# Performance work log

Hardware: AMD Instinct MI355X
Metric: run time of the kernel (lower is better)

The kernel has to match this reference:

```python
import jax, jax.numpy as jnp
import numpy as np
import math

B, L, D, H = 2, 2048, 1024, 16
DH = D // H
TAU = 1.0
EPS_LN = 1e-12


def neural_sort(scores, tau=TAU):
    # scores: (B, n) -> soft permutation P_hat: (B, n, n)
    s = scores[..., None]                                   # (B,n,1)
    A = jnp.abs(s - jnp.swapaxes(s, 1, 2))                  # (B,n,n) pairwise |s_i - s_j|
    Bsum = jnp.sum(A, axis=-1, keepdims=True)               # row sums == A @ ones(n,n) columns
    n = scores.shape[-1]
    scaling = (n + 1 - 2 * (jnp.arange(n) + 1)).astype(scores.dtype)  # (n,)
    C = s * scaling[None, None, :]                          # (B,n,n)
    P_max = jnp.swapaxes(C - Bsum, 1, 2)
    return jax.nn.softmax(P_max / tau, axis=-1)


def euler_transform(v, delta, b_euler, log_scale, is_query):
    # v: (B,L,D); soft-sort channels, polar decompose, rotate, recompose
    Bv, Lv, Dv = v.shape
    scores = v.mean(axis=1)                                 # (B,D)
    P = neural_sort(scores)                                 # (B,D,D)
    v_sorted = jnp.einsum('bij,blj->bli', P, v)             # permute channel dim
    r, p = v_sorted[..., ::2], v_sorted[..., 1::2]          # (B,L,D/2)
    lam = jnp.sqrt(r * r + p * p + 1e-6)
    lam_d = jax.lax.stop_gradient(lam)
    theta = jnp.arctan2(p / lam_d, r / lam_d)
    theta = theta * delta
    if is_query:
        theta = theta + b_euler
    lam = lam * jnp.exp(jnp.clip(log_scale, -5.0, 5.0))
    out = jnp.stack([lam * jnp.cos(theta), lam * jnp.sin(theta)], axis=-1)
    return out.reshape(Bv, Lv, Dv)


def layer_norm(x, gamma, beta, eps=EPS_LN):
    mu = x.mean(axis=-1, keepdims=True)
    var = ((x - mu) ** 2).mean(axis=-1, keepdims=True)
    return (x - mu) / jnp.sqrt(var + eps) * gamma + beta


def forward(input_tensor, Wq, bq, Wk, bk, Wv, bv, Wd, bd, gamma, beta, delta, b_euler, log_scale):
    q = input_tensor @ Wq.T + bq
    k = input_tensor @ Wk.T + bk
    v = input_tensor @ Wv.T + bv
    q = euler_transform(q, delta, b_euler, log_scale, is_query=True)
    k = euler_transform(k, delta, b_euler, log_scale, is_query=False)
    def heads(x):
        return x.reshape(B, L, H, DH).transpose(0, 2, 1, 3)  # (B,H,L,DH)
    qh, kh, vh = heads(q), heads(k), heads(v)
    scores = jnp.einsum('bhqd,bhkd->bhqk', qh, kh) / math.sqrt(DH)
    probs = jax.nn.softmax(scores, axis=-1)                 # dropout off (eval)
    ctx = jnp.einsum('bhqk,bhkd->bhqd', probs, vh)
    ctx = ctx.transpose(0, 2, 1, 3).reshape(B, L, D)
    hidden = ctx @ Wd.T + bd
    return layer_norm(hidden + input_tensor, gamma, beta)


def setup_inputs() -> dict:
    key = jax.random.key(0)
    ks = jax.random.split(key, 16)
    s = 1.0 / math.sqrt(D)
    return {
        'input_tensor': jax.random.normal(ks[0], (B, L, D), jnp.float32),
        'Wq': jax.random.normal(ks[1], (D, D), jnp.float32) * s,
        'bq': jnp.zeros((D,), jnp.float32),
        'Wk': jax.random.normal(ks[2], (D, D), jnp.float32) * s,
        'bk': jnp.zeros((D,), jnp.float32),
        'Wv': jax.random.normal(ks[3], (D, D), jnp.float32) * s,
        'bv': jnp.zeros((D,), jnp.float32),
        'Wd': jax.random.normal(ks[4], (D, D), jnp.float32) * s,
        'bd': jnp.zeros((D,), jnp.float32),
        'gamma': jnp.ones((D,), jnp.float32),
        'beta': jnp.zeros((D,), jnp.float32),
        'delta': jnp.full((1, 1, D // 2), 0.1, jnp.float32),
        'b_euler': jnp.zeros((1, 1, D // 2), jnp.float32),
        'log_scale': jnp.zeros((1, 1, D // 2), jnp.float32),
    }


def reference(input_tensor, Wq, bq, Wk, bk, Wv, bv, Wd, bd, gamma, beta, delta, b_euler, log_scale):
    return forward(input_tensor, Wq, bq, Wk, bk, Wv, bv, Wd, bd, gamma, beta, delta, b_euler, log_scale)
```

## Files before the change

kernel.cpp:

```cpp
#include <hip/hip_runtime.h>


typedef unsigned short bf16_t;
typedef short frag_ab __attribute__((ext_vector_type(8)));
typedef float frag_cd __attribute__((ext_vector_type(4)));

#define BB 2
#define LL 2048
#define DD 1024
#define HH 16
#define DH 64

#define QSCALE 0.18033688f
#define EOFF  -17.3123404907f

__device__ __forceinline__ float b2f(bf16_t u) {
  union { unsigned int i; float f; } c; c.i = ((unsigned int)u) << 16; return c.f;
}
__device__ __forceinline__ bf16_t f2b(float f) {
  union { float f; unsigned int i; } c; c.f = f;
  unsigned int r = c.i + 0x7fffu + ((c.i >> 16) & 1u);
  return (bf16_t)(r >> 16);
}
__device__ __forceinline__ unsigned int fbits(float f) {
  union { float f; unsigned int i; } c; c.f = f; return c.i;
}
__device__ __forceinline__ float tr16(float x) {
  union { float f; unsigned int i; } c; c.f = x; c.i &= 0xffff0000u; return c.f;
}
__device__ __forceinline__ float waveMax(float v) {
#pragma unroll
  for (int m = 32; m > 0; m >>= 1) v = fmaxf(v, __shfl_xor(v, m));
  return v;
}
__device__ __forceinline__ float waveSum(float v) {
#pragma unroll
  for (int m = 32; m > 0; m >>= 1) v += __shfl_xor(v, m);
  return v;
}

__device__ __forceinline__ void gll16(const bf16_t* g, bf16_t* l) {
  __builtin_amdgcn_global_load_lds(
      (const __attribute__((address_space(1))) void*)g,
      (__attribute__((address_space(3))) void*)l, 16, 0, 0);
}

__device__ __forceinline__ frag_ab ld_tile(const bf16_t* base, int row, int chunk) {
  return *(const frag_ab*)((const char*)base + (row << 7) + (((chunk ^ row) & 7) << 4));
}

__global__ __launch_bounds__(256) void prep_cast(const float* __restrict__ X,
                                                 const float* __restrict__ Wv,
                                                 const float* __restrict__ Wd,
                                                 bf16_t* __restrict__ Xb,
                                                 bf16_t* __restrict__ Wvb,
                                                 bf16_t* __restrict__ Wdb,
                                                 float* __restrict__ xmean) {
  const int bid = blockIdx.x;
  if (bid == 6144) {
    if (threadIdx.x < 256)
      for (int i = threadIdx.x; i < BB * DD; i += 256) xmean[i] = 0.f;
    return;
  }
  const float* in;
  bf16_t* out;
  int i;
  if (bid < 4096)      { in = X;  out = Xb;  i = bid * 256 + threadIdx.x; }
  else if (bid < 5120) { in = Wv; out = Wvb; i = (bid - 4096) * 256 + threadIdx.x; }
  else                 { in = Wd; out = Wdb; i = (bid - 5120) * 256 + threadIdx.x; }
  float4 v = ((const float4*)in)[i];
  ushort4 o;
  o.x = f2b(v.x); o.y = f2b(v.y); o.z = f2b(v.z); o.w = f2b(v.w);
  ((ushort4*)out)[i] = o;
}

__global__ __launch_bounds__(256) void cast_transpose_w(const float* __restrict__ Wq,
                                                        const float* __restrict__ Wk,
                                                        bf16_t* __restrict__ WqT,
                                                        bf16_t* __restrict__ WkT) {
  const float* W = blockIdx.z ? Wk : Wq;
  bf16_t* WT = blockIdx.z ? WkT : WqT;
  __shared__ bf16_t T[64][72];
  const int i0 = blockIdx.x * 64, m0 = blockIdx.y * 64;
  const int tid = threadIdx.x;
#pragma unroll
  for (int it = 0; it < 4; ++it) {
    const int idx = tid + it * 256;
    const int r = idx >> 4, c4 = (idx & 15) * 4;
    float4 v = *(const float4*)&W[(size_t)(i0 + r) * DD + m0 + c4];
    T[c4 + 0][r] = f2b(v.x);
    T[c4 + 1][r] = f2b(v.y);
    T[c4 + 2][r] = f2b(v.z);
    T[c4 + 3][r] = f2b(v.w);
  }
  __syncthreads();
#pragma unroll
  for (int it = 0; it < 2; ++it) {
    const int idx = tid + it * 256;
    const int r = idx >> 3, seg = idx & 7;
    *(uint4*)&WT[(size_t)(m0 + r) * DD + i0 + seg * 8] = *(const uint4*)&T[r][seg * 8];
  }
}

struct GemmB { const bf16_t* A; const bf16_t* Bm; const float* bias; float* Cf; bf16_t* Cb; };
struct GemmArgs { GemmB gb[6]; };

__global__ __launch_bounds__(256) void gemm128(GemmArgs ga, int M, int N, int K) {
  const GemmB g = ga.gb[blockIdx.z];
  const int bm = blockIdx.y * 128, bn = blockIdx.x * 128;
  __shared__ bf16_t As[128][32];
  __shared__ bf16_t Bs[128][32];
  bf16_t* As_f = &As[0][0];
  bf16_t* Bs_f = &Bs[0][0];
  const int tid = threadIdx.x;
  const int lane = tid & 63, w = tid >> 6;
  const int quad = lane >> 4, l16 = lane & 15;
  const int wm = (w >> 1) * 64, wn = (w & 1) * 64;
  const int wbase = w << 9;

  frag_cd acc[4][4];
#pragma unroll
  for (int i = 0; i < 4; ++i)
#pragma unroll
    for (int j = 0; j < 4; ++j)
#pragma unroll
      for (int r = 0; r < 4; ++r) acc[i][j][r] = 0.f;

  const int r0 = tid >> 2, s0 = (tid & 3) * 8;
  const int r1 = (tid + 256) >> 2, s1 = ((tid + 256) & 3) * 8;
  const size_t aoff0 = (size_t)(bm + r0) * K + s0;
  const size_t aoff1 = (size_t)(bm + r1) * K + s1;
  const size_t boff0 = (size_t)(bn + r0) * K + s0;
  const size_t boff1 = (size_t)(bn + r1) * K + s1;

  for (int k0 = 0; k0 < K; k0 += 32) {
    __syncthreads();
    gll16(g.A + aoff0 + k0, As_f + wbase);
    gll16(g.A + aoff1 + k0, As_f + 2048 + wbase);
    gll16(g.Bm + boff0 + k0, Bs_f + wbase);
    gll16(g.Bm + boff1 + k0, Bs_f + 2048 + wbase);
    __syncthreads();
    frag_ab af[4], bfr[4];
#pragma unroll
    for (int i = 0; i < 4; ++i) {
      af[i]  = *(const frag_ab*)&As[wm + i * 16 + l16][quad * 8];
      bfr[i] = *(const frag_ab*)&Bs[wn + i * 16 + l16][quad * 8];
    }
#pragma unroll
    for (int i = 0; i < 4; ++i)
#pragma unroll
      for (int j = 0; j < 4; ++j)
        acc[i][j] = __builtin_amdgcn_mfma_f32_16x16x32_bf16(af[i], bfr[j], acc[i][j], 0, 0, 0);
  }

#pragma unroll
  for (int i = 0; i < 4; ++i) {
#pragma unroll
    for (int r = 0; r < 4; ++r) {
      const int row = bm + wm + i * 16 + quad * 4 + r;
#pragma unroll
      for (int j = 0; j < 4; ++j) {
        const int col = bn + wn + j * 16 + l16;
        float v = acc[i][j][r];
        if (g.bias) v += g.bias[col];
        if (g.Cf) g.Cf[(size_t)row * N + col] = v;
        if (g.Cb) g.Cb[(size_t)row * N + col] = f2b(v);
      }
    }
  }
}

__global__ __launch_bounds__(256) void gemm64x64(GemmArgs ga, int M, int N, int K) {
  const GemmB g = ga.gb[blockIdx.z];
  const int bm = blockIdx.y * 64, bn = blockIdx.x * 64;
  __shared__ bf16_t As[64][32];
  __shared__ bf16_t Bs[64][32];
  bf16_t* As_f = &As[0][0];
  bf16_t* Bs_f = &Bs[0][0];
  const int tid = threadIdx.x;
  const int lane = tid & 63, w = tid >> 6;
  const int quad = lane >> 4, l16 = lane & 15;
  const int wm = (w >> 1) * 32, wn = (w & 1) * 32;
  const int wbase = w << 9;

  frag_cd acc[2][2];
#pragma unroll
  for (int i = 0; i < 2; ++i)
#pragma unroll
    for (int j = 0; j < 2; ++j)
#pragma unroll
      for (int r = 0; r < 4; ++r) acc[i][j][r] = 0.f;

  const int r0 = tid >> 2, s0 = (tid & 3) * 8;
  const size_t aoff0 = (size_t)(bm + r0) * K + s0;
  const size_t boff0 = (size_t)(bn + r0) * K + s0;

  for (int k0 = 0; k0 < K; k0 += 32) {
    __syncthreads();
    gll16(g.A + aoff0 + k0, As_f + wbase);
    gll16(g.Bm + boff0 + k0, Bs_f + wbase);
    __syncthreads();
    frag_ab af[2], bfr[2];
#pragma unroll
    for (int i = 0; i < 2; ++i) {
      af[i]  = *(const frag_ab*)&As[wm + i * 16 + l16][quad * 8];
      bfr[i] = *(const frag_ab*)&Bs[wn + i * 16 + l16][quad * 8];
    }
#pragma unroll
    for (int i = 0; i < 2; ++i)
#pragma unroll
      for (int j = 0; j < 2; ++j)
        acc[i][j] = __builtin_amdgcn_mfma_f32_16x16x32_bf16(af[i], bfr[j], acc[i][j], 0, 0, 0);
  }

#pragma unroll
  for (int i = 0; i < 2; ++i) {
#pragma unroll
    for (int r = 0; r < 4; ++r) {
      const int row = bm + wm + i * 16 + quad * 4 + r;
#pragma unroll
      for (int j = 0; j < 2; ++j) {
        const int col = bn + wn + j * 16 + l16;
        float v = acc[i][j][r];
        if (g.bias) v += g.bias[col];
        if (g.Cf) g.Cf[(size_t)row * N + col] = v;
        if (g.Cb) g.Cb[(size_t)row * N + col] = f2b(v);
      }
    }
  }
}

__global__ __launch_bounds__(256) void xmean_kernel(const float* __restrict__ X,
                                                    float* __restrict__ xmean) {
  const int d = blockIdx.x * 256 + threadIdx.x;
  const int b = blockIdx.z;
  const int l0 = blockIdx.y * 64;
  float s = 0.f;
  for (int l = l0; l < l0 + 64; ++l)
    s += X[((size_t)b * LL + l) * DD + d];
  atomicAdd(&xmean[b * DD + d], s * (1.f / (float)LL));
}

__global__ __launch_bounds__(256) void scores_gemm(const float* __restrict__ xmean,
                                                   const float* __restrict__ Wq,
                                                   const float* __restrict__ bq,
                                                   const float* __restrict__ Wk,
                                                   const float* __restrict__ bk,
                                                   float* __restrict__ scores) {
  const int w = threadIdx.x >> 6, lane = threadIdx.x & 63;
  const int idx = blockIdx.x * 4 + w;
  const int t = idx >> 11, b = (idx >> 10) & 1, i = idx & 1023;
  const float* W = t ? Wk : Wq;
  const float* bias = t ? bk : bq;
  const float* xm = xmean + b * DD;
  float sum = 0.f;
#pragma unroll
  for (int k = 0; k < 4; ++k) {
    float4 wv = *(const float4*)&W[(size_t)i * DD + k * 256 + lane * 4];
    float4 xv = *(const float4*)&xm[k * 256 + lane * 4];
    sum += wv.x * xv.x + wv.y * xv.y + wv.z * xv.z + wv.w * xv.w;
  }
  sum = waveSum(sum);
  if (lane == 0) scores[idx] = sum + bias[i];
}

__global__ __launch_bounds__(256) void bsum_kernel(const float* __restrict__ scores,
                                                   float* __restrict__ bsum) {
  __shared__ float sc[DD];
  const int z = blockIdx.x, jb = blockIdx.y, tid = threadIdx.x;
#pragma unroll
  for (int s = 0; s < 4; ++s) sc[tid + s * 256] = scores[z * DD + tid + s * 256];
  __syncthreads();
  const int j = jb * 256 + tid;
  const float si = sc[j];
  float s = 0.f;
  for (int m = 0; m < DD; m += 4) {
    float4 v = *(const float4*)&sc[m];
    s += fabsf(si - v.x) + fabsf(si - v.y) + fabsf(si - v.z) + fabsf(si - v.w);
  }
  bsum[z * DD + j] = s;
}

__global__ __launch_bounds__(256) void p_kernel(const float* __restrict__ scores,
                                                const float* __restrict__ bsum,
                                                const float* __restrict__ bq,
                                                const float* __restrict__ bk,
                                                bf16_t* __restrict__ Pq,
                                                bf16_t* __restrict__ Pk,
                                                float* __restrict__ bias4) {
  const int i = blockIdx.x;
  const int z = blockIdx.y;
  const int t = z >> 1, b = z & 1;
  const float* sc = scores + z * DD;
  const float* bs = bsum + z * DD;
  const float* bias = t ? bk : bq;
  const float scal = 1023.f - 2.f * (float)i;
  const int tid = threadIdx.x;
  __shared__ float redA[4], redB[4], redC[4];

  float lg[4], bb[4];
  float mx = -1e30f;
#pragma unroll
  for (int s = 0; s < 4; ++s) {
    const int j = tid + s * 256;
    lg[s] = sc[j] * scal - bs[j];
    bb[s] = bias[j];
    mx = fmaxf(mx, lg[s]);
  }
  mx = waveMax(mx);
  if ((tid & 63) == 0) redA[tid >> 6] = mx;
  __syncthreads();
  const float M = fmaxf(fmaxf(redA[0], redA[1]), fmaxf(redA[2], redA[3]));
  float sum = 0.f, dot = 0.f;
#pragma unroll
  for (int s = 0; s < 4; ++s) {
    lg[s] = __expf(lg[s] - M);
    sum += lg[s];
    dot += lg[s] * bb[s];
  }
  sum = waveSum(sum); dot = waveSum(dot);
  if ((tid & 63) == 0) { redB[tid >> 6] = sum; redC[tid >> 6] = dot; }
  __syncthreads();
  const float inv = 1.f / (redB[0] + redB[1] + redB[2] + redB[3]);
  bf16_t* P = (t ? Pk : Pq) + ((size_t)b << 20) + (size_t)i * DD;
#pragma unroll
  for (int s = 0; s < 4; ++s) P[tid + s * 256] = f2b(lg[s] * inv);
  if (tid == 0)
    bias4[t * 2048 + b * 1024 + i] = (redC[0] + redC[1] + redC[2] + redC[3]) * inv;
}

__global__ __launch_bounds__(256) void euler_transv(bf16_t* __restrict__ qs,
                                                    bf16_t* __restrict__ ks,
                                                    const float* __restrict__ delta,
                                                    const float* __restrict__ beul,
                                                    const float* __restrict__ lsc,
                                                    const bf16_t* __restrict__ vb,
                                                    bf16_t* __restrict__ vbT) {
  __shared__ bf16_t T[64][72];
  const int bid = blockIdx.x;
  const int tid = threadIdx.x;
  if (bid < 16384) {
    const int isq = (bid < 8192);
    unsigned int* buf = (unsigned int*)(isq ? qs : ks);
    const int idx = (isq ? bid : bid - 8192) * 256 + tid;
    const int c = idx & 511;
    const size_t n = idx >> 9;
    const unsigned int u = buf[n * 512 + c];
    const float r = b2f((bf16_t)(u & 0xffffu));
    const float p = b2f((bf16_t)(u >> 16));
    float lam = sqrtf(r * r + p * p + 1e-6f);
    float th = atan2f(p, r) * delta[c];
    if (isq) th += beul[c];
    lam *= __expf(fminf(fmaxf(lsc[c], -5.f), 5.f));
    if (isq) lam *= QSCALE;
    float sn, cs;
    __sincosf(th, &sn, &cs);
    buf[n * 512 + c] = ((unsigned int)f2b(lam * sn) << 16) | (unsigned int)f2b(lam * cs);
    return;
  }
  const int tb = bid - 16384;
  const int l0 = (tb & 31) * 64, d0 = ((tb >> 5) & 15) * 64, b = tb >> 9;
  for (int i = tid; i < 512; i += 256) {
    const int r = i >> 3, seg = i & 7;
    uint4 v = *(const uint4*)&vb[((size_t)b * LL + l0 + r) * DD + d0 + seg * 8];
    const bf16_t* vs = (const bf16_t*)&v;
#pragma unroll
    for (int j = 0; j < 8; ++j) T[seg * 8 + j][r] = vs[j];
  }
  __syncthreads();
  for (int i = tid; i < 512; i += 256) {
    const int r = i >> 3, seg = i & 7;
    *(uint4*)&vbT[((size_t)b * DD + d0 + r) * LL + l0 + seg * 8] =
        *(const uint4*)&T[r][seg * 8];
  }
}

__global__ __launch_bounds__(128) void attn_kernel(const bf16_t* __restrict__ Q,
                                                   const bf16_t* __restrict__ Kt,
                                                   const bf16_t* __restrict__ VT,
                                                   bf16_t* __restrict__ O) {
  const int bid = blockIdx.x;
  const int swz = (bid & 7) * 128 + (bid >> 3);
  const int g = swz >> 5;
  const int qt = swz & 31;
  const int b = g >> 4, h = g & 15;
  const int q0 = qt * 64;
  const int tid = threadIdx.x, w = tid >> 6, lane = tid & 63;
  const int quad = lane >> 4, l16 = lane & 15;

  __shared__ bf16_t Ks[2][64 * 64];
  __shared__ bf16_t Vs[2][64 * 64];
  __shared__ bf16_t Ps[64 * 64];

  const size_t base = (size_t)b * LL * DD + (size_t)h * DH;
  const size_t vtb = (size_t)(b * DD + h * DH) * LL;

  frag_ab bq[2][2];
#pragma unroll
  for (int qg = 0; qg < 2; ++qg)
#pragma unroll
    for (int kh = 0; kh < 2; ++kh)
      bq[qg][kh] = *(const frag_ab*)
          &Q[base + (size_t)(q0 + w * 32 + qg * 16 + l16) * DD + kh * 32 + quad * 8];

  frag_cd o_[2][4];
#pragma unroll
  for (int qg = 0; qg < 2; ++qg)
#pragma unroll
    for (int n = 0; n < 4; ++n)
#pragma unroll
      for (int r = 0; r < 4; ++r) o_[qg][n][r] = 0.f;
  float ls0 = 0.f, ls1 = 0.f;

  const int srow = lane >> 3;
  const int cg = (lane & 7) ^ srow;
  const int rbase = w * 32;

  auto STAGE = [&](int buf, int kt) {
#pragma unroll
    for (int t = 0; t < 4; ++t) {
      const int row = rbase + t * 8 + srow;
      gll16(Kt + base + (size_t)(kt * 64 + row) * DD + cg * 8,
            &Ks[buf][(rbase + t * 8) * 64]);
      gll16(VT + vtb + (size_t)row * LL + kt * 64 + cg * 8,
            &Vs[buf][(rbase + t * 8) * 64]);
    }
  };

  STAGE(0, 0);
  int cur = 0;
  const int NT = LL / 64;
  for (int kt = 0; kt < NT; ++kt) {
    if (kt + 1 < NT) {
      STAGE(cur ^ 1, kt + 1);
      asm volatile("s_waitcnt vmcnt(8)" ::: "memory");
    } else {
      asm volatile("s_waitcnt vmcnt(0)" ::: "memory");
    }
    __builtin_amdgcn_s_barrier();

    const bf16_t* Kb = Ks[cur];
    const bf16_t* Vb = Vs[cur];

    frag_ab ak[4][2];
#pragma unroll
    for (int n = 0; n < 4; ++n) {
      ak[n][0] = ld_tile(Kb, n * 16 + l16, quad);
      ak[n][1] = ld_tile(Kb, n * 16 + l16, 4 + quad);
    }

#pragma unroll
    for (int qg = 0; qg < 2; ++qg) {
      const int prow = rbase + qg * 16 + l16;
      char* pb = (char*)Ps + prow * 128 + ((quad & 1) << 3);
      float lacc = 0.f;
#pragma unroll
      for (int n = 0; n < 4; ++n) {
        frag_cd z; z[0] = z[1] = z[2] = z[3] = EOFF;
        z = __builtin_amdgcn_mfma_f32_16x16x32_bf16(ak[n][0], bq[qg][0], z, 0, 0, 0);
        z = __builtin_amdgcn_mfma_f32_16x16x32_bf16(ak[n][1], bq[qg][1], z, 0, 0, 0);
        float p0 = __builtin_amdgcn_exp2f(z[0]);
        float p1 = __builtin_amdgcn_exp2f(z[1]);
        float p2 = __builtin_amdgcn_exp2f(z[2]);
        float p3 = __builtin_amdgcn_exp2f(z[3]);
        lacc += (tr16(p0) + tr16(p1)) + (tr16(p2) + tr16(p3));
        unsigned int u01 = __builtin_amdgcn_perm(fbits(p1), fbits(p0), 0x07060302u);
        unsigned int u23 = __builtin_amdgcn_perm(fbits(p3), fbits(p2), 0x07060302u);
        uint2 pk; pk.x = u01; pk.y = u23;
        const int pc = 2 * n + (quad >> 1);
        *(uint2*)(pb + (((pc ^ l16) & 7) << 4)) = pk;
      }
      if (qg == 0) ls0 += lacc; else ls1 += lacc;
    }

    frag_ab ap[2][2];
#pragma unroll
    for (int qg = 0; qg < 2; ++qg) {
      const int prow = rbase + qg * 16 + l16;
      ap[qg][0] = ld_tile(Ps, prow, quad);
      ap[qg][1] = ld_tile(Ps, prow, 4 + quad);
    }
#pragma unroll
    for (int n = 0; n < 4; ++n) {
      frag_ab bv0 = ld_tile(Vb, n * 16 + l16, quad);
      frag_ab bv1 = ld_tile(Vb, n * 16 + l16, 4 + quad);
#pragma unroll
      for (int qg = 0; qg < 2; ++qg) {
        o_[qg][n] = __builtin_amdgcn_mfma_f32_16x16x32_bf16(ap[qg][0], bv0, o_[qg][n], 0, 0, 0);
        o_[qg][n] = __builtin_amdgcn_mfma_f32_16x16x32_bf16(ap[qg][1], bv1, o_[qg][n], 0, 0, 0);
      }
    }
    __builtin_amdgcn_s_barrier();
    cur ^= 1;
  }

#pragma unroll
  for (int qg = 0; qg < 2; ++qg) {
    float l = (qg == 0) ? ls0 : ls1;
    l += __shfl_xor(l, 16);
    l += __shfl_xor(l, 32);
#pragma unroll
    for (int r = 0; r < 4; ++r) {
      const int src = (lane & 48) + ((lane & 48) >> 2) + r;
      const float linv = 1.f / __shfl(l, src);
      const int row = q0 + w * 32 + qg * 16 + quad * 4 + r;
#pragma unroll
      for (int n = 0; n < 4; ++n)
        O[base + (size_t)row * DD + n * 16 + l16] = f2b(o_[qg][n][r] * linv);
    }
  }
}

__global__ __launch_bounds__(256) void ln_kernel(const bf16_t* __restrict__ hidden,
                                                 const float* __restrict__ x0,
                                                 const float* __restrict__ gamma,
                                                 const float* __restrict__ beta,
                                                 float* __restrict__ out) {
  const int row = blockIdx.x;
  const int tid = threadIdx.x;
  __shared__ float red1[4], red2[4];
  float v[4];
  float s1 = 0.f, s2 = 0.f;
#pragma unroll
  for (int s = 0; s < 4; ++s) {
    const int c = tid + s * 256;
    const float x = b2f(hidden[(size_t)row * DD + c]) + x0[(size_t)row * DD + c];
    v[s] = x; s1 += x; s2 += x * x;
  }
  s1 = waveSum(s1); s2 = waveSum(s2);
  if ((tid & 63) == 0) { red1[tid >> 6] = s1; red2[tid >> 6] = s2; }
  __syncthreads();
  const float t1 = red1[0] + red1[1] + red1[2] + red1[3];
  const float t2 = red2[0] + red2[1] + red2[2] + red2[3];
  const float mu = t1 * (1.f / DD);
  const float var = t2 * (1.f / DD) - mu * mu;
  const float inv = rsqrtf(var + 1e-12f);
#pragma unroll
  for (int s = 0; s < 4; ++s) {
    const int c = tid + s * 256;
    out[(size_t)row * DD + c] = (v[s] - mu) * inv * gamma[c] + beta[c];
  }
}

extern "C" void kernel_launch(void* const* d_in, const int* in_sizes, int n_in,
                              void* d_out, int out_size, void* d_ws, size_t ws_size,
                              hipStream_t stream) {
  const float* X    = (const float*)d_in[0];
  const float* Wq   = (const float*)d_in[1];
  const float* bq   = (const float*)d_in[2];
  const float* Wk   = (const float*)d_in[3];
  const float* bk   = (const float*)d_in[4];
  const float* Wv   = (const float*)d_in[5];
  const float* bv   = (const float*)d_in[6];
  const float* Wd   = (const float*)d_in[7];
  const float* bd   = (const float*)d_in[8];
  const float* gam  = (const float*)d_in[9];
  const float* bet  = (const float*)d_in[10];
  const float* delt = (const float*)d_in[11];
  const float* beul = (const float*)d_in[12];
  const float* lsc  = (const float*)d_in[13];
  float* out = (float*)d_out;

  char* w = (char*)d_ws;
  const size_t MB = 1024ull * 1024ull;
  bf16_t* Xb  = (bf16_t*)(w + 0 * MB);
  bf16_t* Wvb = (bf16_t*)(w + 8 * MB);
  bf16_t* Wdb = (bf16_t*)(w + 10 * MB);
  bf16_t* WqT = (bf16_t*)(w + 12 * MB);
  bf16_t* WkT = (bf16_t*)(w + 14 * MB);
  bf16_t* Pq  = (bf16_t*)(w + 16 * MB);
  bf16_t* Pk  = (bf16_t*)(w + 20 * MB);
  bf16_t* Wp  = (bf16_t*)(w + 24 * MB);
  bf16_t* vb  = (bf16_t*)(w + 32 * MB);
  bf16_t* qs  = (bf16_t*)(w + 40 * MB);
  bf16_t* ks  = (bf16_t*)(w + 48 * MB);
  bf16_t* vbT = (bf16_t*)(w + 56 * MB);
  bf16_t* ctx = (bf16_t*)(w + 64 * MB);
  bf16_t* hid = (bf16_t*)(w + 24 * MB);
  float*  xmean  = (float*)(w + 72 * MB);
  float*  scores = (float*)(w + 72 * MB + 16384);
  float*  bsum   = (float*)(w + 72 * MB + 32768);
  float*  bias4  = (float*)(w + 72 * MB + 49152);

  const size_t WSZ = (size_t)DD * DD;

  prep_cast<<<dim3(6145), 256, 0, stream>>>(X, Wv, Wd, Xb, Wvb, Wdb, xmean);
  cast_transpose_w<<<dim3(16, 16, 2), 256, 0, stream>>>(Wq, Wk, WqT, WkT);

  xmean_kernel<<<dim3(4, 32, 2), 256, 0, stream>>>(X, xmean);
  scores_gemm<<<dim3(1024), 256, 0, stream>>>(xmean, Wq, bq, Wk, bk, scores);

  bsum_kernel<<<dim3(4, 4), 256, 0, stream>>>(scores, bsum);
  p_kernel<<<dim3(1024, 4), 256, 0, stream>>>(scores, bsum, bq, bk, Pq, Pk, bias4);

  GemmArgs gw = {};
  gw.gb[0] = {Pq,       WqT, nullptr, nullptr, Wp};
  gw.gb[1] = {Pq + WSZ, WqT, nullptr, nullptr, Wp + WSZ};
  gw.gb[2] = {Pk,       WkT, nullptr, nullptr, Wp + 2 * WSZ};
  gw.gb[3] = {Pk + WSZ, WkT, nullptr, nullptr, Wp + 3 * WSZ};
  gemm64x64<<<dim3(16, 16, 4), 256, 0, stream>>>(gw, DD, DD, DD);

  const size_t XHALF = (size_t)LL * DD;
  GemmArgs gs = {};
  gs.gb[0] = {Xb,         Wp,           bias4,        nullptr, qs};
  gs.gb[1] = {Xb + XHALF, Wp + WSZ,     bias4 + 1024, nullptr, qs + XHALF};
  gs.gb[2] = {Xb,         Wp + 2 * WSZ, bias4 + 2048, nullptr, ks};
  gs.gb[3] = {Xb + XHALF, Wp + 3 * WSZ, bias4 + 3072, nullptr, ks + XHALF};
  gs.gb[4] = {Xb,         Wvb,          bv,           nullptr, vb};
  gs.gb[5] = {Xb + XHALF, Wvb,          bv,           nullptr, vb + XHALF};
  gemm128<<<dim3(8, 16, 6), 256, 0, stream>>>(gs, LL, DD, DD);

  euler_transv<<<dim3(17408), 256, 0, stream>>>(qs, ks, delt, beul, lsc, vb, vbT);

  attn_kernel<<<dim3(1024), 128, 0, stream>>>(qs, ks, vbT, ctx);

  GemmArgs g4 = {};
  g4.gb[0] = {ctx, Wdb, bd, nullptr, hid};
  gemm64x64<<<dim3(16, 64, 1), 256, 0, stream>>>(g4, BB * LL, DD, DD);

  ln_kernel<<<dim3(BB * LL), 256, 0, stream>>>(hid, X, gam, bet, out);
}
```

Before: 311.0 us.

## Split attention across four waves and compute row sums via MFMA

The attention kernel now launches 256 threads per block, so each wave handles 16 query rows instead of 32. Each wave's share of the K/V tile staging shrinks to match. The softmax denominator is no longer accumulated with truncation and VALU adds. It is now computed by an extra MFMA that multiplies the bf16 probability tile by a ones-column fragment. This cuts per-wave register and VALU work and raises parallelism, at the cost of more waves contending for the same LDS tiles and barriers.

```diff
diff --git a/kernel.cpp b/kernel.cpp
--- a/kernel.cpp
+++ b/kernel.cpp
@@ -24,9 +24,6 @@
 }
 __device__ __forceinline__ unsigned int fbits(float f) {
   union { float f; unsigned int i; } c; c.f = f; return c.i;
-}
-__device__ __forceinline__ float tr16(float x) {
-  union { float f; unsigned int i; } c; c.f = x; c.i &= 0xffff0000u; return c.f;
 }
 __device__ __forceinline__ float waveMax(float v) {
 #pragma unroll
@@ -375,7 +372,7 @@
   }
 }
 
-__global__ __launch_bounds__(128) void attn_kernel(const bf16_t* __restrict__ Q,
+__global__ __launch_bounds__(256) void attn_kernel(const bf16_t* __restrict__ Q,
                                                    const bf16_t* __restrict__ Kt,
                                                    const bf16_t* __restrict__ VT,
                                                    bf16_t* __restrict__ O) {
@@ -395,30 +392,33 @@
   const size_t base = (size_t)b * LL * DD + (size_t)h * DH;
   const size_t vtb = (size_t)(b * DD + h * DH) * LL;
 
-  frag_ab bq[2][2];
-#pragma unroll
-  for (int qg = 0; qg < 2; ++qg)
-#pragma unroll
-    for (int kh = 0; kh < 2; ++kh)
-      bq[qg][kh] = *(const frag_ab*)
-          &Q[base + (size_t)(q0 + w * 32 + qg * 16 + l16) * DD + kh * 32 + quad * 8];
-
-  frag_cd o_[2][4];
-#pragma unroll
-  for (int qg = 0; qg < 2; ++qg)
-#pragma unroll
-    for (int n = 0; n < 4; ++n)
-#pragma unroll
-      for (int r = 0; r < 4; ++r) o_[qg][n][r] = 0.f;
-  float ls0 = 0.f, ls1 = 0.f;
+  frag_ab bq0 = *(const frag_ab*)
+      &Q[base + (size_t)(q0 + w * 16 + l16) * DD + quad * 8];
+  frag_ab bq1 = *(const frag_ab*)
+      &Q[base + (size_t)(q0 + w * 16 + l16) * DD + 32 + quad * 8];
+
+  frag_ab bone;
+  {
+    const short o = (l16 == 0) ? (short)0x3F80 : (short)0;
+#pragma unroll
+    for (int j = 0; j < 8; ++j) bone[j] = o;
+  }
+
+  frag_cd o_[4], l5;
+#pragma unroll
+  for (int n = 0; n < 4; ++n)
+#pragma unroll
+    for (int r = 0; r < 4; ++r) o_[n][r] = 0.f;
+#pragma unroll
+  for (int r = 0; r < 4; ++r) l5[r] = 0.f;
 
   const int srow = lane >> 3;
   const int cg = (lane & 7) ^ srow;
-  const int rbase = w * 32;
+  const int rbase = w * 16;
 
   auto STAGE = [&](int buf, int kt) {
 #pragma unroll
-    for (int t = 0; t < 4; ++t) {
+    for (int t = 0; t < 2; ++t) {
       const int row = rbase + t * 8 + srow;
       gll16(Kt + base + (size_t)(kt * 64 + row) * DD + cg * 8,
             &Ks[buf][(rbase + t * 8) * 64]);
@@ -433,7 +433,7 @@
   for (int kt = 0; kt < NT; ++kt) {
     if (kt + 1 < NT) {
       STAGE(cur ^ 1, kt + 1);
-      asm volatile("s_waitcnt vmcnt(8)" ::: "memory");
+      asm volatile("s_waitcnt vmcnt(4)" ::: "memory");
     } else {
       asm volatile("s_waitcnt vmcnt(0)" ::: "memory");
     }
@@ -449,66 +449,52 @@
       ak[n][1] = ld_tile(Kb, n * 16 + l16, 4 + quad);
     }
 
-#pragma unroll
-    for (int qg = 0; qg < 2; ++qg) {
-      const int prow = rbase + qg * 16 + l16;
-      char* pb = (char*)Ps + prow * 128 + ((quad & 1) << 3);
-      float lacc = 0.f;
-#pragma unroll
-      for (int n = 0; n < 4; ++n) {
-        frag_cd z; z[0] = z[1] = z[2] = z[3] = EOFF;
-        z = __builtin_amdgcn_mfma_f32_16x16x32_bf16(ak[n][0], bq[qg][0], z, 0, 0, 0);
-        z = __builtin_amdgcn_mfma_f32_16x16x32_bf16(ak[n][1], bq[qg][1], z, 0, 0, 0);
-        float p0 = __builtin_amdgcn_exp2f(z[0]);
-        float p1 = __builtin_amdgcn_exp2f(z[1]);
-        float p2 = __builtin_amdgcn_exp2f(z[2]);
-        float p3 = __builtin_amdgcn_exp2f(z[3]);
-        lacc += (tr16(p0) + tr16(p1)) + (tr16(p2) + tr16(p3));
-        unsigned int u01 = __builtin_amdgcn_perm(fbits(p1), fbits(p0), 0x07060302u);
-        unsigned int u23 = __builtin_amdgcn_perm(fbits(p3), fbits(p2), 0x07060302u);
-        uint2 pk; pk.x = u01; pk.y = u23;
-        const int pc = 2 * n + (quad >> 1);
-        *(uint2*)(pb + (((pc ^ l16) & 7) << 4)) = pk;
-      }
-      if (qg == 0) ls0 += lacc; else ls1 += lacc;
-    }
-
-    frag_ab ap[2][2];
-#pragma unroll
-    for (int qg = 0; qg < 2; ++qg) {
-      const int prow = rbase + qg * 16 + l16;
-      ap[qg][0] = ld_tile(Ps, prow, quad);
-      ap[qg][1] = ld_tile(Ps, prow, 4 + quad);
-    }
+    const int prow = rbase + l16;
+    char* pb = (char*)Ps + prow * 128 + ((quad & 1) << 3);
+#pragma unroll
+    for (int n = 0; n < 4; ++n) {
+      frag_cd z; z[0] = z[1] = z[2] = z[3] = EOFF;
+      z = __builtin_amdgcn_mfma_f32_16x16x32_bf16(ak[n][0], bq0, z, 0, 0, 0);
+      z = __builtin_amdgcn_mfma_f32_16x16x32_bf16(ak[n][1], bq1, z, 0, 0, 0);
+      float p0 = __builtin_amdgcn_exp2f(z[0]);
+      float p1 = __builtin_amdgcn_exp2f(z[1]);
+      float p2 = __builtin_amdgcn_exp2f(z[2]);
+      float p3 = __builtin_amdgcn_exp2f(z[3]);
+      unsigned int u01 = __builtin_amdgcn_perm(fbits(p1), fbits(p0), 0x07060302u);
+      unsigned int u23 = __builtin_amdgcn_perm(fbits(p3), fbits(p2), 0x07060302u);
+      uint2 pk; pk.x = u01; pk.y = u23;
+      const int pc = 2 * n + (quad >> 1);
+      *(uint2*)(pb + (((pc ^ l16) & 7) << 4)) = pk;
+    }
+
+    frag_ab ap0 = ld_tile(Ps, prow, quad);
+    frag_ab ap1 = ld_tile(Ps, prow, 4 + quad);
+
+    l5 = __builtin_amdgcn_mfma_f32_16x16x32_bf16(ap0, bone, l5, 0, 0, 0);
+    l5 = __builtin_amdgcn_mfma_f32_16x16x32_bf16(ap1, bone, l5, 0, 0, 0);
+
 #pragma unroll
     for (int n = 0; n < 4; ++n) {
       frag_ab bv0 = ld_tile(Vb, n * 16 + l16, quad);
       frag_ab bv1 = ld_tile(Vb, n * 16 + l16, 4 + quad);
-#pragma unroll
-      for (int qg = 0; qg < 2; ++qg) {
-        o_[qg][n] = __builtin_amdgcn_mfma_f32_16x16x32_bf16(ap[qg][0], bv0, o_[qg][n], 0, 0, 0);
-        o_[qg][n] = __builtin_amdgcn_mfma_f32_16x16x32_bf16(ap[qg][1], bv1, o_[qg][n], 0, 0, 0);
-      }
+      o_[n] = __builtin_amdgcn_mfma_f32_16x16x32_bf16(ap0, bv0, o_[n], 0, 0, 0);
+      o_[n] = __builtin_amdgcn_mfma_f32_16x16x32_bf16(ap1, bv1, o_[n], 0, 0, 0);
     }
     __builtin_amdgcn_s_barrier();
     cur ^= 1;
   }
 
-#pragma unroll
-  for (int qg = 0; qg < 2; ++qg) {
-    float l = (qg == 0) ? ls0 : ls1;
-    l += __shfl_xor(l, 16);
-    l += __shfl_xor(l, 32);
+  float lfin[4];
+#pragma unroll
+  for (int r = 0; r < 4; ++r) lfin[r] = 1.f / __shfl(l5[r], quad << 4);
+
+#pragma unroll
+  for (int n = 0; n < 4; ++n)
 #pragma unroll
     for (int r = 0; r < 4; ++r) {
-      const int src = (lane & 48) + ((lane & 48) >> 2) + r;
-      const float linv = 1.f / __shfl(l, src);
-      const int row = q0 + w * 32 + qg * 16 + quad * 4 + r;
-#pragma unroll
-      for (int n = 0; n < 4; ++n)
-        O[base + (size_t)row * DD + n * 16 + l16] = f2b(o_[qg][n][r] * linv);
-    }
-  }
+      const float v = o_[n][r] * lfin[r];
+      O[base + (size_t)(q0 + w * 16 + quad * 4 + r) * DD + n * 16 + l16] = f2b(v);
+    }
 }
 
 __global__ __launch_bounds__(256) void ln_kernel(const bf16_t* __restrict__ hidden,
@@ -612,7 +598,7 @@
 
   euler_transv<<<dim3(17408), 256, 0, stream>>>(qs, ks, delt, beul, lsc, vb, vbT);
 
-  attn_kernel<<<dim3(1024), 128, 0, stream>>>(qs, ks, vbT, ctx);
+  attn_kernel<<<dim3(1024), 256, 0, stream>>>(qs, ks, vbT, ctx);
 
   GemmArgs g4 = {};
   g4.gb[0] = {ctx, Wdb, bd, nullptr, hid};
```

After: 297.9 us. 4.2% less time.
